# Optimization experiments

Hardware: AMD Instinct MI355X
Metric: run time of the kernel (lower is better)

Reference implementation:

```python
import jax, jax.numpy as jnp
import numpy as np
from jax import lax

K = 3  # AdaConv kernel_size inside conv_block


def conv2d(x, w, b, pad):
    # x: (B,C,H,W), w: (O,I,kh,kw) -> NCHW conv with symmetric padding
    y = lax.conv_general_dilated(x, w, (1, 1), [(pad, pad), (pad, pad)],
                                 dimension_numbers=('NCHW', 'OIHW', 'NCHW'))
    return y + b[None, :, None, None]


def unfold3(x):
    # nn.Unfold(kernel=3, pad=1): patches ordered channel-major then (kh,kw) row-major
    B, C, H, W = x.shape
    xp = jnp.pad(x, ((0, 0), (0, 0), (1, 1), (1, 1)))
    return jnp.stack([xp[:, :, i:i + H, j:j + W]
                      for i in range(K) for j in range(K)], axis=2)  # (B,C,9,H,W)


def adaconv(x, mask, aw_w, aw_b, mt_w, mt_b, c_w, c_b):
    # groups=1, groups_channels=out_ch in this configuration
    weight = conv2d(mask, aw_w, aw_b, pad=2)          # (B, 9, H, W)
    x = conv2d(x, c_w, c_b, pad=1)                    # (B, out_ch, H, W)
    p = unfold3(x)                                    # (B, out_ch, 9, H, W)
    out = jnp.einsum('bkhw,bckhw->bchw', weight, p)   # per-pixel adaptive conv
    mask2 = conv2d(mask, mt_w, mt_b, pad=2)
    return out, mask2


def lrelu(x):
    return jax.nn.leaky_relu(x, 0.01)


def setup_inputs() -> dict:
    key = jax.random.key(0)
    ks = jax.random.split(key, 20)
    B, Cin, Cout, Mi, Mo, H, W = 2, 64, 64, 64, 64, 256, 256
    s = 0.05
    d = {
        'x': jax.random.normal(ks[0], (B, Cin, H, W), jnp.float32),
        'mask': jax.random.normal(ks[1], (B, Mi, H, W), jnp.float32),
        # AdaConv 1 (in_ch->out_ch, mask_in->mask_out)
        'aw1_w': jax.random.normal(ks[2], (K * K, Mi, 2 * K - 1, 2 * K - 1), jnp.float32) * s,
        'aw1_b': jax.random.normal(ks[3], (K * K,), jnp.float32) * s,
        'mt1_w': jax.random.normal(ks[4], (Mo, Mi, 2 * K - 1, 2 * K - 1), jnp.float32) * s,
        'mt1_b': jax.random.normal(ks[5], (Mo,), jnp.float32) * s,
        'c1_w': jax.random.normal(ks[6], (Cout, Cin, K, K), jnp.float32) * s,
        'c1_b': jax.random.normal(ks[7], (Cout,), jnp.float32) * s,
        # AdaConv 2 (out_ch->out_ch, mask_out->mask_out)
        'aw2_w': jax.random.normal(ks[8], (K * K, Mo, 2 * K - 1, 2 * K - 1), jnp.float32) * s,
        'aw2_b': jax.random.normal(ks[9], (K * K,), jnp.float32) * s,
        'mt2_w': jax.random.normal(ks[10], (Mo, Mo, 2 * K - 1, 2 * K - 1), jnp.float32) * s,
        'mt2_b': jax.random.normal(ks[11], (Mo,), jnp.float32) * s,
        'c2_w': jax.random.normal(ks[12], (Cout, Cout, K, K), jnp.float32) * s,
        'c2_b': jax.random.normal(ks[13], (Cout,), jnp.float32) * s,
        # 1x1 residual conv
        'cr_w': jax.random.normal(ks[14], (Cout, Cin, 1, 1), jnp.float32) * s,
        'cr_b': jax.random.normal(ks[15], (Cout,), jnp.float32) * s,
    }
    return d


def reference(x, mask, aw1_w, aw1_b, mt1_w, mt1_b, c1_w, c1_b,
              aw2_w, aw2_b, mt2_w, mt2_b, c2_w, c2_b, cr_w, cr_b):
    res = conv2d(x, cr_w, cr_b, pad=0)
    x, mask = adaconv(x, mask, aw1_w, aw1_b, mt1_w, mt1_b, c1_w, c1_b)
    x, mask = lrelu(x), lrelu(mask)
    x, mask = adaconv(x, mask, aw2_w, aw2_b, mt2_w, mt2_b, c2_w, c2_b)
    x, mask = lrelu(x), lrelu(mask)
    return (x + res, mask)
```

## Files before the change

### kernel.cpp

```cpp
#include <hip/hip_runtime.h>

#define HWSZ 65536
#define CCH  64

typedef __bf16 bf16x8 __attribute__((ext_vector_type(8)));
typedef __bf16 bf16x4 __attribute__((ext_vector_type(4)));
typedef float  f32x4  __attribute__((ext_vector_type(4)));

__device__ inline void gload_lds16(const void* g, void* l) {
    __builtin_amdgcn_global_load_lds(
        (const __attribute__((address_space(1))) void*)g,
        (__attribute__((address_space(3))) void*)l, 16, 0, 0);
}


__device__ void cvt_body(int cb, const float* __restrict__ src,
                         __bf16* __restrict__ dst)
{
    int p  = cb * 256 + threadIdx.x;
    int b  = p >> 16, hw = p & 65535;
    const float* sp = src + (((size_t)b * 64) << 16) + hw;
    __bf16* dp = dst + (size_t)p * 64;
    #pragma unroll
    for (int c8 = 0; c8 < 8; ++c8) {
        bf16x8 v8;
        #pragma unroll
        for (int j = 0; j < 8; ++j)
            v8[j] = (__bf16)sp[(size_t)(c8 * 8 + j) << 16];
        *(bf16x8*)(dp + c8 * 8) = v8;
    }
}

__device__ void prep3_body(int cb, const float* __restrict__ src,
                           __bf16* __restrict__ dst)
{
    int t = cb * 256 + threadIdx.x;
    if (t >= 2 * 9 * 2048) return;
    int j  = t & 7;
    int u  = (t >> 3) & 255;
    int q  = t >> 11;
    int k  = q % 9, ci = q / 9;
    int r  = u >> 3;
    int v  = (u & 7) ^ (r & 7);
    int o  = 2 * r + (v >> 2);
    int g  = v & 3;
    int i  = ci * 32 + g * 8 + j;
    dst[t] = (__bf16)src[((size_t)o * 64 + i) * 9 + k];
}

__device__ void prepF_body(int cb, const float* __restrict__ mt,
                           const float* __restrict__ aw, __bf16* __restrict__ dst)
{
    int t = cb * 256 + threadIdx.x;
    if (t >= 2 * 25 * 3072) return;
    int j  = t & 7;
    int u  = (t >> 3) % 384;
    int q  = t / 3072;
    int k  = q % 25, ci = q / 25;
    int r  = u >> 3;
    int v  = (u & 7) ^ (r & 7);
    int o  = 2 * r + (v >> 2);
    int g  = v & 3;
    int i  = ci * 32 + g * 8 + j;
    float val = 0.f;
    if (o < 64)      val = mt[((size_t)o * 64 + i) * 25 + k];
    else if (o < 73) val = aw[((size_t)(o - 64) * 64 + i) * 25 + k];
    dst[t] = (__bf16)val;
}

__global__ __launch_bounds__(256) void k_prep(
    const float* x, const float* mask,
    const float* c1w, const float* c2w,
    const float* mt1w, const float* aw1w,
    const float* mt2w, const float* aw2w,
    __bf16* xh, __bf16* mh,
    __bf16* wbc1, __bf16* wbc2, __bf16* wbF1, __bf16* wbF2)
{
    int bid = blockIdx.x;
    if      (bid < 512)  cvt_body(bid, x, xh);
    else if (bid < 1024) cvt_body(bid - 512, mask, mh);
    else if (bid < 1168) prep3_body(bid - 1024, c1w, wbc1);
    else if (bid < 1312) prep3_body(bid - 1168, c2w, wbc2);
    else if (bid < 1912) prepF_body(bid - 1312, mt1w, aw1w, wbF1);
    else                 prepF_body(bid - 1912, mt2w, aw2w, wbF2);
}

template<int KSZ, int MFT, int RELU, int EPI>
__global__ __launch_bounds__(256) void k_mconv(
    const __bf16* __restrict__ xh, const __bf16* __restrict__ wb,
    const float* __restrict__ bias, const float* __restrict__ bias2,
    float* __restrict__ outf, __bf16* __restrict__ outh,
    float* __restrict__ out2)
{
    constexpr int PAD   = KSZ / 2;
    constexpr int TW    = 16 + 2 * PAD;
    constexpr int NPIX  = TW * TW;
    constexpr int KK    = KSZ * KSZ;
    constexpr int SROWS = (MFT == 5) ? 96 : 64;
    constexpr int SLICE = SROWS * 64;
    constexpr int NPIX2 = NPIX / 2;

    __shared__ __align__(16) __bf16 lx[NPIX2 * 64];
    __shared__ __align__(16) __bf16 lw[2][SROWS * 32];
    __shared__ float lb[80];

    const int t    = threadIdx.x;
    const int w0   = blockIdx.x * 16, h0 = blockIdx.y * 16, b = blockIdx.z;
    const int wvv  = t >> 6;
    const int lane = t & 63;
    const int px   = lane & 15;
    const int g    = lane >> 4;

    auto STAGE = [&](int ci, int k, int buf) {
        const char* gs = (const char*)wb + (size_t)(ci * KK + k) * SLICE;
        char* lbase = (char*)lw[buf];
        if constexpr (MFT == 5) {
            if (wvv < 3) {
                #pragma unroll
                for (int r = 0; r < 2; ++r) {
                    int ub = wvv * 128 + r * 64;
                    gload_lds16(gs + (ub + lane) * 16, lbase + ub * 16);
                }
            }
        } else {
            int ub = wvv * 64;
            gload_lds16(gs + (ub + lane) * 16, lbase + ub * 16);
        }
    };

    f32x4 acc[MFT][4];
    #pragma unroll
    for (int m = 0; m < MFT; ++m)
        #pragma unroll
        for (int nf = 0; nf < 4; ++nf)
            acc[m][nf] = (f32x4){0.f, 0.f, 0.f, 0.f};

    bf16x8 zv;
    #pragma unroll
    for (int j = 0; j < 8; ++j) zv[j] = (__bf16)0.f;

    for (int ci = 0; ci < 2; ++ci) {
        if (ci) __syncthreads();
        STAGE(ci, 0, 0);
        STAGE(ci, 1, 1);
        if (ci == 0) {
            if (t < 64) lb[t] = bias[t];
            if constexpr (MFT == 5) {
                if (t >= 64 && t < 80) lb[t] = (t - 64 < 9) ? bias2[t - 64] : 0.f;
            }
        }

        constexpr int XITER = (NPIX * 4 + 255) / 256;
        #pragma unroll
        for (int xi = 0; xi < XITER; ++xi) {
            int e = xi * 256 + t;
            if (e < NPIX * 4) {
                int pix = e >> 2, c4 = e & 3;
                int sy = pix / TW, sx = pix - sy * TW;
                int gy = h0 + sy - PAD, gx = w0 + sx - PAD;
                bool ok = (unsigned)gy < 256u && (unsigned)gx < 256u;
                bf16x8 v8 = zv;
                if (ok) v8 = *(const bf16x8*)(xh + ((((size_t)b << 16) + gy * 256 + gx) << 6)
                                              + ci * 32 + c4 * 8);
                int row = pix >> 1;
                int off = row * 128 + (((((pix & 1) << 2) + c4) ^ (row & 7)) << 4);
                *(bf16x8*)((char*)lx + off) = v8;
            }
        }
        __syncthreads();

        #pragma unroll
        for (int k = 0; k < KK; ++k) {
            const __bf16* lwb = lw[k & 1];
            const int dy = k / KSZ, dx = k - dy * KSZ;

            bf16x8 bfr[4];
            #pragma unroll
            for (int nf = 0; nf < 4; ++nf) {
                int pix = (wvv * 4 + nf + dy) * TW + (px + dx);
                int row = pix >> 1;
                int off = row * 128 + (((((pix & 1) << 2) + g) ^ (row & 7)) << 4);
                bfr[nf] = *(const bf16x8*)((const char*)lx + off);
            }
            bf16x8 afr[MFT];
            #pragma unroll
            for (int m = 0; m < MFT; ++m) {
                int o = m * 16 + px;
                int row = o >> 1;
                int off = row * 128 + (((((o & 1) << 2) + g) ^ (row & 7)) << 4);
                afr[m] = *(const bf16x8*)((const char*)lwb + off);
            }
            __builtin_amdgcn_s_setprio(1);
            #pragma unroll
            for (int m = 0; m < MFT; ++m)
                #pragma unroll
                for (int nf = 0; nf < 4; ++nf)
                    acc[m][nf] = __builtin_amdgcn_mfma_f32_16x16x32_bf16(
                        afr[m], bfr[nf], acc[m][nf], 0, 0, 0);
            __builtin_amdgcn_s_setprio(0);

            if (k == KK - 1) break;

            asm volatile("s_waitcnt lgkmcnt(0)" ::: "memory");
            __builtin_amdgcn_sched_barrier(0);
            __builtin_amdgcn_s_barrier();
            bool issued = (k + 2 < KK);
            if (issued) STAGE(ci, k + 2, k & 1);
            if constexpr (MFT == 5) {
                if (issued && wvv < 3) asm volatile("s_waitcnt vmcnt(2)" ::: "memory");
                else                   asm volatile("s_waitcnt vmcnt(0)" ::: "memory");
            } else {
                if (issued) asm volatile("s_waitcnt vmcnt(1)" ::: "memory");
                else        asm volatile("s_waitcnt vmcnt(0)" ::: "memory");
            }
            __builtin_amdgcn_sched_barrier(0);
            __builtin_amdgcn_s_barrier();
        }
    }

    #pragma unroll
    for (int m = 0; m < MFT; ++m) {
        #pragma unroll
        for (int nf = 0; nf < 4; ++nf) {
            int row = h0 + wvv * 4 + nf, col = w0 + px;
            if (m < 4) {
                float vj[4];
                #pragma unroll
                for (int j = 0; j < 4; ++j) {
                    float v = acc[m][nf][j] + lb[m * 16 + g * 4 + j];
                    if (RELU) v = v > 0.f ? v : 0.01f * v;
                    vj[j] = v;
                }
                if constexpr (EPI == 0) {
                    bf16x4 pk;
                    #pragma unroll
                    for (int j = 0; j < 4; ++j) pk[j] = (__bf16)vj[j];
                    *(bf16x4*)(outh + ((((size_t)b << 16) + row * 256 + col) << 6)
                                    + m * 16 + g * 4) = pk;
                } else {
                    #pragma unroll
                    for (int j = 0; j < 4; ++j)
                        outf[((size_t)(b * 64 + m * 16 + g * 4 + j) << 16)
                             + row * 256 + col] = vj[j];
                }
            } else {
                #pragma unroll
                for (int j = 0; j < 4; ++j) {
                    int o2 = g * 4 + j;
                    if (o2 < 9)
                        out2[((size_t)(b * 9 + o2) << 16) + row * 256 + col]
                            = acc[m][nf][j] + lb[64 + o2];
                }
            }
        }
    }
}

__global__ __launch_bounds__(256) void k_conv1x1(
    const __bf16* __restrict__ xh, const float* __restrict__ w,
    const float* __restrict__ bias, float* __restrict__ out)
{
    __shared__ __align__(16) float lwT[4096];
    __shared__ float lb[64];
    int t = threadIdx.x;
    for (int s = t; s < 4096; s += 256) lwT[s] = w[(s & 63) * 64 + (s >> 6)];
    if (t < 64) lb[t] = bias[t];
    __syncthreads();

    int p  = blockIdx.x * 256 + t;
    int b  = p >> 16, hw = p & 65535;
    const __bf16* xp = xh + (size_t)p * 64;

    float acc[64];
    #pragma unroll
    for (int o = 0; o < 64; ++o) acc[o] = lb[o];

    #pragma unroll
    for (int c8 = 0; c8 < 8; ++c8) {
        bf16x8 v8 = *(const bf16x8*)(xp + c8 * 8);
        #pragma unroll
        for (int j = 0; j < 8; ++j) {
            float xi = (float)v8[j];
            const float4* w4 = (const float4*)&lwT[(c8 * 8 + j) * 64];
            #pragma unroll
            for (int o4 = 0; o4 < 16; ++o4) {
                float4 wv = w4[o4];
                acc[o4*4+0] += wv.x * xi;
                acc[o4*4+1] += wv.y * xi;
                acc[o4*4+2] += wv.z * xi;
                acc[o4*4+3] += wv.w * xi;
            }
        }
    }
    float* op = out + (((size_t)b * 64) << 16) + hw;
    #pragma unroll
    for (int o = 0; o < 64; ++o) op[(size_t)o << 16] = acc[o];
}

__global__ __launch_bounds__(256, 4) void k_ada1(
    const float* __restrict__ wgt, const __bf16* __restrict__ xin,
    __bf16* __restrict__ outh)
{
    int t  = threadIdx.x;
    int pg = t >> 3, c8 = t & 7;
    int p  = blockIdx.x * 32 + pg;
    int b  = p >> 16, hw = p & 65535;
    int h  = hw >> 8, wc = hw & 255;

    const float* wp = wgt + ((size_t)(b * 9) << 16) + hw;
    const __bf16* cen = xin + (size_t)p * 64 + c8 * 8;

    float wk[9];
    const __bf16* nbp[9];
    #pragma unroll
    for (int dy = 0; dy < 3; ++dy)
        #pragma unroll
        for (int dx = 0; dx < 3; ++dx) {
            int k = dy * 3 + dx;
            bool ok = ((unsigned)(h + dy - 1) < 256u) &&
                      ((unsigned)(wc + dx - 1) < 256u);
            wk[k]  = ok ? wp[(size_t)k << 16] : 0.f;
            nbp[k] = ok ? cen + ((dy - 1) * 256 + (dx - 1)) * 64 : cen;
        }

    float acc[8] = {0.f,0.f,0.f,0.f,0.f,0.f,0.f,0.f};
    #pragma unroll
    for (int k = 0; k < 9; ++k) {
        bf16x8 v8 = *(const bf16x8*)nbp[k];
        float w = wk[k];
        #pragma unroll
        for (int j = 0; j < 8; ++j) acc[j] += w * (float)v8[j];
    }

    bf16x8 o8;
    #pragma unroll
    for (int j = 0; j < 8; ++j) {
        float v = acc[j];
        o8[j] = (__bf16)(v > 0.f ? v : 0.01f * v);
    }
    *(bf16x8*)(outh + (size_t)p * 64 + c8 * 8) = o8;
}

__global__ __launch_bounds__(256, 4) void k_ada2(
    const float* __restrict__ wgt, const __bf16* __restrict__ x2h,
    float* __restrict__ outf)
{
    __shared__ float ls[32 * 65];

    int t  = threadIdx.x;
    int pg = t >> 3, c8 = t & 7;
    int p  = blockIdx.x * 32 + pg;
    int b  = p >> 16, hw = p & 65535;
    int h  = hw >> 8, wc = hw & 255;

    const float* wp = wgt + ((size_t)(b * 9) << 16) + hw;
    const __bf16* cen = x2h + (size_t)p * 64 + c8 * 8;

    float wk[9];
    const __bf16* nbp[9];
    #pragma unroll
    for (int dy = 0; dy < 3; ++dy)
        #pragma unroll
        for (int dx = 0; dx < 3; ++dx) {
            int k = dy * 3 + dx;
            bool ok = ((unsigned)(h + dy - 1) < 256u) &&
                      ((unsigned)(wc + dx - 1) < 256u);
            wk[k]  = ok ? wp[(size_t)k << 16] : 0.f;
            nbp[k] = ok ? cen + ((dy - 1) * 256 + (dx - 1)) * 64 : cen;
        }

    float acc[8] = {0.f,0.f,0.f,0.f,0.f,0.f,0.f,0.f};
    #pragma unroll
    for (int k = 0; k < 9; ++k) {
        bf16x8 v8 = *(const bf16x8*)nbp[k];
        float w = wk[k];
        #pragma unroll
        for (int j = 0; j < 8; ++j) acc[j] += w * (float)v8[j];
    }

    #pragma unroll
    for (int j = 0; j < 8; ++j) {
        float v = acc[j];
        ls[pg * 65 + c8 * 8 + j] = v > 0.f ? v : 0.01f * v;
    }
    __syncthreads();

    int pbase = blockIdx.x * 32;
    int bb    = pbase >> 16, hwb = pbase & 65535;
    int pix   = t & 31, cq = t >> 5;
    #pragma unroll
    for (int i = 0; i < 8; ++i) {
        int c = i * 8 + cq;
        float v = ls[pix * 65 + c];
        float* op = outf + ((size_t)(bb * 64 + c) << 16) + hwb + pix;
        *op = *op + v;
    }
}

extern "C" void kernel_launch(void* const* d_in, const int* in_sizes, int n_in,
                              void* d_out, int out_size, void* d_ws, size_t ws_size,
                              hipStream_t stream)
{
    const float* x     = (const float*)d_in[0];
    const float* mask  = (const float*)d_in[1];
    const float* aw1_w = (const float*)d_in[2];
    const float* aw1_b = (const float*)d_in[3];
    const float* mt1_w = (const float*)d_in[4];
    const float* mt1_b = (const float*)d_in[5];
    const float* c1_w  = (const float*)d_in[6];
    const float* c1_b  = (const float*)d_in[7];
    const float* aw2_w = (const float*)d_in[8];
    const float* aw2_b = (const float*)d_in[9];
    const float* mt2_w = (const float*)d_in[10];
    const float* mt2_b = (const float*)d_in[11];
    const float* c2_w  = (const float*)d_in[12];
    const float* c2_b  = (const float*)d_in[13];
    const float* cr_w  = (const float*)d_in[14];
    const float* cr_b  = (const float*)d_in[15];

    float* out_x = (float*)d_out;
    float* out_m = (float*)d_out + 8388608;

    float*  wgt   = (float*)d_ws;
    __bf16* xh    = (__bf16*)((char*)d_ws + 4718592);
    __bf16* mh    = (__bf16*)((char*)d_ws + 21495808);
    __bf16* x2h   = mh;
    __bf16* wbase = (__bf16*)((char*)d_ws + 38273024);
    __bf16* wb_c1 = wbase;
    __bf16* wb_c2 = wbase + 36864;
    __bf16* wb_F1 = wbase + 73728;
    __bf16* wb_F2 = wbase + 227328;

    __bf16* maska_h = (__bf16*)out_x;
    __bf16* xa_h    = (__bf16*)out_x + 8388608;
    __bf16* x1_h    = (__bf16*)out_m;

    dim3 blk(256);
    dim3 gconv(16, 16, 2);
    dim3 gpix(512);
    dim3 gada(4096);

    k_prep<<<dim3(2512), blk, 0, stream>>>(x, mask, c1_w, c2_w,
        mt1_w, aw1_w, mt2_w, aw2_w, xh, mh, wb_c1, wb_c2, wb_F1, wb_F2);

    k_mconv<5,5,1,0><<<gconv, blk, 0, stream>>>(mh, wb_F1, mt1_b, aw1_b,
                                                nullptr, maska_h, wgt);
    k_mconv<3,4,0,0><<<gconv, blk, 0, stream>>>(xh, wb_c1, c1_b, nullptr,
                                                nullptr, x1_h, nullptr);
    k_ada1<<<gada, blk, 0, stream>>>(wgt, x1_h, xa_h);
    k_mconv<5,5,1,1><<<gconv, blk, 0, stream>>>(maska_h, wb_F2, mt2_b, aw2_b,
                                                out_m, nullptr, wgt);
    k_mconv<3,4,0,0><<<gconv, blk, 0, stream>>>(xa_h, wb_c2, c2_b, nullptr,
                                                nullptr, x2h, nullptr);
    k_conv1x1<<<gpix, blk, 0, stream>>>(xh, cr_w, cr_b, out_x);
    k_ada2<<<gada, blk, 0, stream>>>(wgt, x2h, out_x);
}
```

Measured before the change: 196.9 us.

## Fuse 1x1 residual conv into prep, store bf16 residual, specialize 3x3 conv

The 1x1 residual conv moves into the prep kernel, reads the fp32 input directly, and writes a bf16 residual buffer. The final adaptive-conv kernel then adds that residual instead of doing a read-modify-write on the fp32 output, so one launch goes away. The 3x3 conv gets its own kernel that stages all 9 weight slices into LDS at once, replacing per-tap double buffering with barriers, and the 5x5 kernel is specialized. The cost is that the residual is stored at bf16 precision, the prep kernel grows and uses 16KB of shared memory for every block, and the 1x1 body reads fp32 at a 256KB channel stride.

```diff
diff --git a/kernel.cpp b/kernel.cpp
--- a/kernel.cpp
+++ b/kernel.cpp
@@ -68,37 +68,75 @@
     dst[t] = (__bf16)val;
 }
 
+__device__ void conv1x1p_body(float* lwT, float* lb, int cb,
+    const float* __restrict__ x, const float* __restrict__ w,
+    const float* __restrict__ bias, __bf16* __restrict__ res)
+{
+    int t = threadIdx.x;
+    for (int s = t; s < 4096; s += 256) lwT[s] = w[(s & 63) * 64 + (s >> 6)];
+    if (t < 64) lb[t] = bias[t];
+    __syncthreads();
+
+    int p  = cb * 256 + t;
+    int b  = p >> 16, hw = p & 65535;
+    const float* xp = x + (((size_t)b * 64) << 16) + hw;
+
+    float acc[64];
+    #pragma unroll
+    for (int o = 0; o < 64; ++o) acc[o] = lb[o];
+
+    #pragma unroll 4
+    for (int i = 0; i < 64; ++i) {
+        float xi = xp[(size_t)i << 16];
+        const float4* w4 = (const float4*)&lwT[i * 64];
+        #pragma unroll
+        for (int o4 = 0; o4 < 16; ++o4) {
+            float4 wv = w4[o4];
+            acc[o4*4+0] += wv.x * xi;
+            acc[o4*4+1] += wv.y * xi;
+            acc[o4*4+2] += wv.z * xi;
+            acc[o4*4+3] += wv.w * xi;
+        }
+    }
+    __bf16* op = res + (((size_t)b * 64) << 16) + hw;
+    #pragma unroll
+    for (int o = 0; o < 64; ++o) op[(size_t)o << 16] = (__bf16)acc[o];
+}
+
 __global__ __launch_bounds__(256) void k_prep(
     const float* x, const float* mask,
     const float* c1w, const float* c2w,
     const float* mt1w, const float* aw1w,
     const float* mt2w, const float* aw2w,
-    __bf16* xh, __bf16* mh,
+    const float* crw, const float* crb,
+    __bf16* xh, __bf16* mh, __bf16* resh,
     __bf16* wbc1, __bf16* wbc2, __bf16* wbF1, __bf16* wbF2)
 {
+    __shared__ __align__(16) float s1x1[4160];
     int bid = blockIdx.x;
-    if      (bid < 512)  cvt_body(bid, x, xh);
-    else if (bid < 1024) cvt_body(bid - 512, mask, mh);
-    else if (bid < 1168) prep3_body(bid - 1024, c1w, wbc1);
-    else if (bid < 1312) prep3_body(bid - 1168, c2w, wbc2);
-    else if (bid < 1912) prepF_body(bid - 1312, mt1w, aw1w, wbF1);
-    else                 prepF_body(bid - 1912, mt2w, aw2w, wbF2);
-}
-
-template<int KSZ, int MFT, int RELU, int EPI>
-__global__ __launch_bounds__(256) void k_mconv(
+    if      (bid < 512)  conv1x1p_body(s1x1, s1x1 + 4096, bid, x, crw, crb, resh);
+    else if (bid < 1024) cvt_body(bid - 512, x, xh);
+    else if (bid < 1536) cvt_body(bid - 1024, mask, mh);
+    else if (bid < 1680) prep3_body(bid - 1536, c1w, wbc1);
+    else if (bid < 1824) prep3_body(bid - 1680, c2w, wbc2);
+    else if (bid < 2424) prepF_body(bid - 1824, mt1w, aw1w, wbF1);
+    else                 prepF_body(bid - 2424, mt2w, aw2w, wbF2);
+}
+
+template<int EPI>
+__global__ __launch_bounds__(256) void k_conv5(
     const __bf16* __restrict__ xh, const __bf16* __restrict__ wb,
     const float* __restrict__ bias, const float* __restrict__ bias2,
     float* __restrict__ outf, __bf16* __restrict__ outh,
     float* __restrict__ out2)
 {
-    constexpr int PAD   = KSZ / 2;
-    constexpr int TW    = 16 + 2 * PAD;
-    constexpr int NPIX  = TW * TW;
-    constexpr int KK    = KSZ * KSZ;
-    constexpr int SROWS = (MFT == 5) ? 96 : 64;
+    constexpr int TW    = 20;
+    constexpr int NPIX  = 400;
+    constexpr int KK    = 25;
+    constexpr int SROWS = 96;
     constexpr int SLICE = SROWS * 64;
     constexpr int NPIX2 = NPIX / 2;
+    constexpr int MFT   = 5;
 
     __shared__ __align__(16) __bf16 lx[NPIX2 * 64];
     __shared__ __align__(16) __bf16 lw[2][SROWS * 32];
@@ -113,18 +151,12 @@
 
     auto STAGE = [&](int ci, int k, int buf) {
         const char* gs = (const char*)wb + (size_t)(ci * KK + k) * SLICE;
-        char* lbase = (char*)lw[buf];
-        if constexpr (MFT == 5) {
-            if (wvv < 3) {
-                #pragma unroll
-                for (int r = 0; r < 2; ++r) {
-                    int ub = wvv * 128 + r * 64;
-                    gload_lds16(gs + (ub + lane) * 16, lbase + ub * 16);
-                }
-            }
-        } else {
-            int ub = wvv * 64;
-            gload_lds16(gs + (ub + lane) * 16, lbase + ub * 16);
+        if (wvv < 3) {
+            #pragma unroll
+            for (int r = 0; r < 2; ++r) {
+                int ub = wvv * 128 + r * 64;
+                gload_lds16(gs + (ub + lane) * 16, (char*)lw[buf] + ub * 16);
+            }
         }
     };
 
@@ -145,19 +177,16 @@
         STAGE(ci, 1, 1);
         if (ci == 0) {
             if (t < 64) lb[t] = bias[t];
-            if constexpr (MFT == 5) {
-                if (t >= 64 && t < 80) lb[t] = (t - 64 < 9) ? bias2[t - 64] : 0.f;
-            }
-        }
-
-        constexpr int XITER = (NPIX * 4 + 255) / 256;
-        #pragma unroll
-        for (int xi = 0; xi < XITER; ++xi) {
+            if (t >= 64 && t < 80) lb[t] = (t - 64 < 9) ? bias2[t - 64] : 0.f;
+        }
+
+        #pragma unroll
+        for (int xi = 0; xi < 7; ++xi) {
             int e = xi * 256 + t;
             if (e < NPIX * 4) {
                 int pix = e >> 2, c4 = e & 3;
                 int sy = pix / TW, sx = pix - sy * TW;
-                int gy = h0 + sy - PAD, gx = w0 + sx - PAD;
+                int gy = h0 + sy - 2, gx = w0 + sx - 2;
                 bool ok = (unsigned)gy < 256u && (unsigned)gx < 256u;
                 bf16x8 v8 = zv;
                 if (ok) v8 = *(const bf16x8*)(xh + ((((size_t)b << 16) + gy * 256 + gx) << 6)
@@ -171,8 +200,8 @@
 
         #pragma unroll
         for (int k = 0; k < KK; ++k) {
-            const __bf16* lwb = lw[k & 1];
-            const int dy = k / KSZ, dx = k - dy * KSZ;
+            const __bf16* lwb = (k & 1) ? lw[1] : lw[0];
+            const int dy = k / 5, dx = k - dy * 5;
 
             bf16x8 bfr[4];
             #pragma unroll
@@ -206,13 +235,8 @@
             __builtin_amdgcn_s_barrier();
             bool issued = (k + 2 < KK);
             if (issued) STAGE(ci, k + 2, k & 1);
-            if constexpr (MFT == 5) {
-                if (issued && wvv < 3) asm volatile("s_waitcnt vmcnt(2)" ::: "memory");
-                else                   asm volatile("s_waitcnt vmcnt(0)" ::: "memory");
-            } else {
-                if (issued) asm volatile("s_waitcnt vmcnt(1)" ::: "memory");
-                else        asm volatile("s_waitcnt vmcnt(0)" ::: "memory");
-            }
+            if (issued && wvv < 3) asm volatile("s_waitcnt vmcnt(2)" ::: "memory");
+            else                   asm volatile("s_waitcnt vmcnt(0)" ::: "memory");
             __builtin_amdgcn_sched_barrier(0);
             __builtin_amdgcn_s_barrier();
         }
@@ -228,8 +252,7 @@
                 #pragma unroll
                 for (int j = 0; j < 4; ++j) {
                     float v = acc[m][nf][j] + lb[m * 16 + g * 4 + j];
-                    if (RELU) v = v > 0.f ? v : 0.01f * v;
-                    vj[j] = v;
+                    vj[j] = v > 0.f ? v : 0.01f * v;
                 }
                 if constexpr (EPI == 0) {
                     bf16x4 pk;
@@ -256,45 +279,113 @@
     }
 }
 
-__global__ __launch_bounds__(256) void k_conv1x1(
-    const __bf16* __restrict__ xh, const float* __restrict__ w,
-    const float* __restrict__ bias, float* __restrict__ out)
-{
-    __shared__ __align__(16) float lwT[4096];
+__global__ __launch_bounds__(256) void k_conv3(
+    const __bf16* __restrict__ xh, const __bf16* __restrict__ wb,
+    const float* __restrict__ bias, __bf16* __restrict__ outh)
+{
+    constexpr int TW    = 18;
+    constexpr int NPIX  = 324;
+    constexpr int NPIX2 = 162;
+
+    __shared__ __align__(16) __bf16 lx[NPIX2 * 64];
+    __shared__ __align__(16) __bf16 lw[9 * 2048];
     __shared__ float lb[64];
-    int t = threadIdx.x;
-    for (int s = t; s < 4096; s += 256) lwT[s] = w[(s & 63) * 64 + (s >> 6)];
-    if (t < 64) lb[t] = bias[t];
-    __syncthreads();
-
-    int p  = blockIdx.x * 256 + t;
-    int b  = p >> 16, hw = p & 65535;
-    const __bf16* xp = xh + (size_t)p * 64;
-
-    float acc[64];
-    #pragma unroll
-    for (int o = 0; o < 64; ++o) acc[o] = lb[o];
-
-    #pragma unroll
-    for (int c8 = 0; c8 < 8; ++c8) {
-        bf16x8 v8 = *(const bf16x8*)(xp + c8 * 8);
-        #pragma unroll
-        for (int j = 0; j < 8; ++j) {
-            float xi = (float)v8[j];
-            const float4* w4 = (const float4*)&lwT[(c8 * 8 + j) * 64];
-            #pragma unroll
-            for (int o4 = 0; o4 < 16; ++o4) {
-                float4 wv = w4[o4];
-                acc[o4*4+0] += wv.x * xi;
-                acc[o4*4+1] += wv.y * xi;
-                acc[o4*4+2] += wv.z * xi;
-                acc[o4*4+3] += wv.w * xi;
-            }
-        }
-    }
-    float* op = out + (((size_t)b * 64) << 16) + hw;
-    #pragma unroll
-    for (int o = 0; o < 64; ++o) op[(size_t)o << 16] = acc[o];
+
+    const int t    = threadIdx.x;
+    const int w0   = blockIdx.x * 16, h0 = blockIdx.y * 16, b = blockIdx.z;
+    const int wvv  = t >> 6;
+    const int lane = t & 63;
+    const int px   = lane & 15;
+    const int g    = lane >> 4;
+
+    f32x4 acc[4][4];
+    #pragma unroll
+    for (int m = 0; m < 4; ++m)
+        #pragma unroll
+        for (int nf = 0; nf < 4; ++nf)
+            acc[m][nf] = (f32x4){0.f, 0.f, 0.f, 0.f};
+
+    bf16x8 zv;
+    #pragma unroll
+    for (int j = 0; j < 8; ++j) zv[j] = (__bf16)0.f;
+
+    for (int ci = 0; ci < 2; ++ci) {
+        if (ci) __syncthreads();
+        {
+            const char* gs = (const char*)wb + (size_t)ci * 9 * 4096;
+            #pragma unroll
+            for (int r = 0; r < 9; ++r) {
+                int ub = r * 256 + wvv * 64;
+                gload_lds16(gs + (ub + lane) * 16, (char*)lw + ub * 16);
+            }
+        }
+        if (ci == 0 && t < 64) lb[t] = bias[t];
+
+        #pragma unroll
+        for (int xi = 0; xi < 6; ++xi) {
+            int e = xi * 256 + t;
+            if (e < NPIX * 4) {
+                int pix = e >> 2, c4 = e & 3;
+                int sy = pix / TW, sx = pix - sy * TW;
+                int gy = h0 + sy - 1, gx = w0 + sx - 1;
+                bool ok = (unsigned)gy < 256u && (unsigned)gx < 256u;
+                bf16x8 v8 = zv;
+                if (ok) v8 = *(const bf16x8*)(xh + ((((size_t)b << 16) + gy * 256 + gx) << 6)
+                                              + ci * 32 + c4 * 8);
+                int row = pix >> 1;
+                int off = row * 128 + (((((pix & 1) << 2) + c4) ^ (row & 7)) << 4);
+                *(bf16x8*)((char*)lx + off) = v8;
+            }
+        }
+        __syncthreads();
+
+        #pragma unroll
+        for (int k = 0; k < 9; ++k) {
+            const __bf16* lwb = lw + k * 2048;
+            const int dy = k / 3, dx = k - dy * 3;
+
+            bf16x8 bfr[4];
+            #pragma unroll
+            for (int nf = 0; nf < 4; ++nf) {
+                int pix = (wvv * 4 + nf + dy) * TW + (px + dx);
+                int row = pix >> 1;
+                int off = row * 128 + (((((pix & 1) << 2) + g) ^ (row & 7)) << 4);
+                bfr[nf] = *(const bf16x8*)((const char*)lx + off);
+            }
+            bf16x8 afr[4];
+            #pragma unroll
+            for (int m = 0; m < 4; ++m) {
+                int o = m * 16 + px;
+                int row = o >> 1;
+                int off = row * 128 + (((((o & 1) << 2) + g) ^ (row & 7)) << 4);
+                afr[m] = *(const bf16x8*)((const char*)lwb + off);
+            }
+            __builtin_amdgcn_s_setprio(1);
+            #pragma unroll
+            for (int m = 0; m < 4; ++m)
+                #pragma unroll
+                for (int nf = 0; nf < 4; ++nf)
+                    acc[m][nf] = __builtin_amdgcn_mfma_f32_16x16x32_bf16(
+                        afr[m], bfr[nf], acc[m][nf], 0, 0, 0);
+            __builtin_amdgcn_s_setprio(0);
+        }
+    }
+
+    #pragma unroll
+    for (int m = 0; m < 4; ++m) {
+        #pragma unroll
+        for (int nf = 0; nf < 4; ++nf) {
+            int row = h0 + wvv * 4 + nf, col = w0 + px;
+            bf16x4 pk;
+            #pragma unroll
+            for (int j = 0; j < 4; ++j) {
+                float v = acc[m][nf][j] + lb[m * 16 + g * 4 + j];
+                pk[j] = (__bf16)v;
+            }
+            *(bf16x4*)(outh + ((((size_t)b << 16) + row * 256 + col) << 6)
+                            + m * 16 + g * 4) = pk;
+        }
+    }
 }
 
 __global__ __launch_bounds__(256, 4) void k_ada1(
@@ -343,7 +434,7 @@
 
 __global__ __launch_bounds__(256, 4) void k_ada2(
     const float* __restrict__ wgt, const __bf16* __restrict__ x2h,
-    float* __restrict__ outf)
+    const __bf16* __restrict__ resh, float* __restrict__ outf)
 {
     __shared__ float ls[32 * 65];
 
@@ -391,9 +482,8 @@
     #pragma unroll
     for (int i = 0; i < 8; ++i) {
         int c = i * 8 + cq;
-        float v = ls[pix * 65 + c];
-        float* op = outf + ((size_t)(bb * 64 + c) << 16) + hwb + pix;
-        *op = *op + v;
+        size_t oi = ((size_t)(bb * 64 + c) << 16) + hwb + pix;
+        outf[oi] = ls[pix * 65 + c] + (float)resh[oi];
     }
 }
 
@@ -430,6 +520,7 @@
     __bf16* wb_c2 = wbase + 36864;
     __bf16* wb_F1 = wbase + 73728;
     __bf16* wb_F2 = wbase + 227328;
+    __bf16* resh  = (__bf16*)((char*)d_ws + 39034880);
 
     __bf16* maska_h = (__bf16*)out_x;
     __bf16* xa_h    = (__bf16*)out_x + 8388608;
@@ -437,21 +528,18 @@
 
     dim3 blk(256);
     dim3 gconv(16, 16, 2);
-    dim3 gpix(512);
     dim3 gada(4096);
 
-    k_prep<<<dim3(2512), blk, 0, stream>>>(x, mask, c1_w, c2_w,
-        mt1_w, aw1_w, mt2_w, aw2_w, xh, mh, wb_c1, wb_c2, wb_F1, wb_F2);
-
-    k_mconv<5,5,1,0><<<gconv, blk, 0, stream>>>(mh, wb_F1, mt1_b, aw1_b,
-                                                nullptr, maska_h, wgt);
-    k_mconv<3,4,0,0><<<gconv, blk, 0, stream>>>(xh, wb_c1, c1_b, nullptr,
-                                                nullptr, x1_h, nullptr);
+    k_prep<<<dim3(3024), blk, 0, stream>>>(x, mask, c1_w, c2_w,
+        mt1_w, aw1_w, mt2_w, aw2_w, cr_w, cr_b,
+        xh, mh, resh, wb_c1, wb_c2, wb_F1, wb_F2);
+
+    k_conv5<0><<<gconv, blk, 0, stream>>>(mh, wb_F1, mt1_b, aw1_b,
+                                          nullptr, maska_h, wgt);
+    k_conv3<<<gconv, blk, 0, stream>>>(xh, wb_c1, c1_b, x1_h);
     k_ada1<<<gada, blk, 0, stream>>>(wgt, x1_h, xa_h);
-    k_mconv<5,5,1,1><<<gconv, blk, 0, stream>>>(maska_h, wb_F2, mt2_b, aw2_b,
-                                                out_m, nullptr, wgt);
-    k_mconv<3,4,0,0><<<gconv, blk, 0, stream>>>(xa_h, wb_c2, c2_b, nullptr,
-                                                nullptr, x2h, nullptr);
-    k_conv1x1<<<gpix, blk, 0, stream>>>(xh, cr_w, cr_b, out_x);
-    k_ada2<<<gada, blk, 0, stream>>>(wgt, x2h, out_x);
-}
+    k_conv5<1><<<gconv, blk, 0, stream>>>(maska_h, wb_F2, mt2_b, aw2_b,
+                                          out_m, nullptr, wgt);
+    k_conv3<<<gconv, blk, 0, stream>>>(xa_h, wb_c2, c2_b, x2h);
+    k_ada2<<<gada, blk, 0, stream>>>(wgt, x2h, resh, out_x);
+}
```

New measurement: 186.3 us. 5.4% less time.
